# Optimization experiments

Measured on AMD Instinct MI355X. Metric: run time of the kernel, lower is better.

Reference implementation:

```python
import jax, jax.numpy as jnp
import numpy as np

N_NODES = 50000
N_EDGES = 600000
IN_DIM = 128
HID = 128
OUT_DIM = 40
NUM_REL = 3
LN_EPS = 1e-5


def layer_norm(x, g, b):
    mu = jnp.mean(x, axis=-1, keepdims=True)
    var = jnp.var(x, axis=-1, keepdims=True)
    return (x - mu) * jax.lax.rsqrt(var + LN_EPS) * g + b


def rgcn_conv(x, edge_index, edge_type, w_rel, w_root, bias, aggr):
    """PyG-style RGCNConv: out = x @ W_root + bias + sum_r aggr_r(x_src @ W_r)."""
    src, dst = edge_index[0], edge_index[1]
    out = x @ w_root + bias                      # [N, F_out]
    for r in range(NUM_REL):                     # small fixed relation loop
        h = x @ w_rel[r]                         # transform-then-gather: [N, F_out]
        msg = h[src]                             # [E, F_out]
        mask = (edge_type == r)[:, None]
        if aggr == 'add':
            msg = jnp.where(mask, msg, 0.0)
            agg = jax.ops.segment_sum(msg, dst, num_segments=N_NODES)
        else:  # 'max'; empty segments -> 0 (matches PyG scatter_reduce include_self=False over zeros)
            msg = jnp.where(mask, msg, -jnp.inf)
            agg = jax.ops.segment_max(msg, dst, num_segments=N_NODES)
            agg = jnp.where(jnp.isfinite(agg), agg, 0.0)
        out = out + agg
    return out


def setup_inputs() -> dict:
    key = jax.random.key(0)
    ks = jax.random.split(key, 16)
    f32 = jnp.float32
    def lin(k, fan_in, shape):
        return jax.random.normal(k, shape, dtype=f32) / np.sqrt(fan_in)
    inp = {
        'x': jax.random.normal(ks[0], (N_NODES, IN_DIM), dtype=f32),
        'edge_index': jax.random.randint(ks[1], (2, N_EDGES), 0, N_NODES),
        'edge_type': jax.random.randint(ks[2], (N_EDGES,), 0, NUM_REL),
        # conv1
        'w1_rel': lin(ks[3], IN_DIM, (NUM_REL, IN_DIM, HID)),
        'w1_root': lin(ks[4], IN_DIM, (IN_DIM, HID)),
        'b1': jnp.zeros((HID,), f32),
        'ln1_g': jnp.ones((HID,), f32), 'ln1_b': jnp.zeros((HID,), f32),
        # conv2
        'w2_rel': lin(ks[5], HID, (NUM_REL, HID, HID)),
        'w2_root': lin(ks[6], HID, (HID, HID)),
        'b2': jnp.zeros((HID,), f32),
        'ln2_g': jnp.ones((HID,), f32), 'ln2_b': jnp.zeros((HID,), f32),
        # classifier
        'cw1': lin(ks[7], HID, (HID, HID)), 'cb1': jnp.zeros((HID,), f32),
        'cln1_g': jnp.ones((HID,), f32), 'cln1_b': jnp.zeros((HID,), f32),
        'cw2': lin(ks[8], HID, (HID, HID // 2)), 'cb2': jnp.zeros((HID // 2,), f32),
        'cln2_g': jnp.ones((HID // 2,), f32), 'cln2_b': jnp.zeros((HID // 2,), f32),
        'cw3': lin(ks[9], HID // 2, (HID // 2, OUT_DIM)), 'cb3': jnp.zeros((OUT_DIM,), f32),
    }
    return inp


def reference(x, edge_index, edge_type,
              w1_rel, w1_root, b1, ln1_g, ln1_b,
              w2_rel, w2_root, b2, ln2_g, ln2_b,
              cw1, cb1, cln1_g, cln1_b,
              cw2, cb2, cln2_g, cln2_b,
              cw3, cb3):
    # eval mode: edge dropout and feature dropout are identity
    h = rgcn_conv(x, edge_index, edge_type, w1_rel, w1_root, b1, 'add')
    h = jax.nn.relu(layer_norm(h, ln1_g, ln1_b))
    x1 = h
    h = rgcn_conv(x1, edge_index, edge_type, w2_rel, w2_root, b2, 'max')
    h = jax.nn.relu(layer_norm(h, ln2_g, ln2_b))
    h = h + x1 * 0.2
    # classifier MLP
    h = jax.nn.gelu(layer_norm(h @ cw1 + cb1, cln1_g, cln1_b), approximate=False)
    h = jax.nn.gelu(layer_norm(h @ cw2 + cb2, cln2_g, cln2_b), approximate=False)
    h = h @ cw3 + cb3
    return jax.nn.log_softmax(h, axis=1)
```

## Files before the change

### kernel.cpp

```cpp
#include <hip/hip_runtime.h>
#include <hip/hip_bf16.h>
#include <math.h>


typedef __attribute__((ext_vector_type(8))) short bf16x8;
typedef __attribute__((ext_vector_type(4))) float f32x4;
typedef unsigned short ushort_t;

__device__ __forceinline__ ushort_t bf16rne(float v) {
    unsigned u = __float_as_uint(v);
    return (ushort_t)((u + 0x7FFFu + ((u >> 16) & 1u)) >> 16);
}

__device__ __forceinline__ void split_bf16(float v, ushort_t& h, ushort_t& l) {
    ushort_t hu = bf16rne(v);
    float hf = __uint_as_float((unsigned)hu << 16);
    h = hu;
    l = bf16rne(v - hf);
}

__device__ __forceinline__ float bf2f(unsigned u16) {
    return __uint_as_float(u16 << 16);
}

__device__ __forceinline__ float4 unpack_bf4(uint2 u) {
    return make_float4(bf2f(u.x & 0xFFFFu), bf2f(u.x >> 16),
                       bf2f(u.y & 0xFFFFu), bf2f(u.y >> 16));
}

__device__ __forceinline__ uint2 pack_bf4(float4 v) {
    uint2 o;
    o.x = (unsigned)bf16rne(v.x) | ((unsigned)bf16rne(v.y) << 16);
    o.y = (unsigned)bf16rne(v.z) | ((unsigned)bf16rne(v.w) << 16);
    return o;
}

__device__ __forceinline__ void conv_body128(const float* __restrict__ W,
                                             ushort_t* __restrict__ out,
                                             int idx) {
    constexpr int NCF = 8;
    constexpr size_t PST = (size_t)4 * NCF * 512;
    int l = idx & 63;
    int cf = (idx >> 6) & 7;
    int ks = idx >> 9;
    int col = cf * 16 + (l & 15);
    int k0 = ks * 32 + (l >> 4) * 8;
    size_t base = (((size_t)ks * NCF + cf) * 64 + l) * 8;
#pragma unroll
    for (int j = 0; j < 8; ++j) {
        ushort_t h, lo_;
        split_bf16(W[(size_t)(k0 + j) * 128 + col], h, lo_);
        out[base + j] = h;
        out[PST + base + j] = lo_;
    }
}

__global__ __launch_bounds__(256) void convert_all_x2bf(
    const float* __restrict__ w1_root, const float* __restrict__ w1_rel,
    const float* __restrict__ w2_root, const float* __restrict__ w2_rel,
    const float* __restrict__ cw1, const float* __restrict__ cw2,
    ushort_t* __restrict__ wfb,
    const float* __restrict__ x, ushort_t* __restrict__ xh, int n4) {
    int b = blockIdx.x;
    if (b >= 76) {
        int g = (b - 76) * 256 + threadIdx.x;
        if (g < n4) {
            float4 v = ((const float4*)x)[g];
            ((uint2*)xh)[g] = pack_bf4(v);
        }
        return;
    }
    if (b < 72) {
        const float* src;
        int slot;
        if (b < 8)       { slot = 0;              src = w1_root; }
        else if (b < 32) { int r = (b - 8) >> 3;  slot = 1 + r; src = w1_rel + (size_t)r * 16384; }
        else if (b < 40) { slot = 4;              src = w2_root; }
        else if (b < 64) { int r = (b - 40) >> 3; slot = 5 + r; src = w2_rel + (size_t)r * 16384; }
        else             { slot = 8;              src = cw1; }
        int lb = (b < 8) ? b : (b < 32) ? ((b - 8) & 7) : (b < 40) ? (b - 32)
               : (b < 64) ? ((b - 40) & 7) : (b - 64);
        conv_body128(src, wfb + (size_t)slot * 32768, lb * 256 + threadIdx.x);
    } else {
        constexpr int NCF = 4;
        constexpr size_t PST = (size_t)4 * NCF * 512;
        int idx = (b - 72) * 256 + threadIdx.x;
        ushort_t* out = wfb + (size_t)9 * 32768;
        int l = idx & 63;
        int cf = (idx >> 6) & 3;
        int ks = idx >> 8;
        int col = cf * 16 + (l & 15);
        int k0 = ks * 32 + (l >> 4) * 8;
        size_t base = (((size_t)ks * NCF + cf) * 64 + l) * 8;
#pragma unroll
        for (int j = 0; j < 8; ++j) {
            ushort_t h, lo_;
            split_bf16(cw2[(size_t)(k0 + j) * 64 + col], h, lo_);
            out[base + j] = h;
            out[PST + base + j] = lo_;
        }
    }
}

template <int NCOL, int NSEG, int FUSE>
__global__ __launch_bounds__(256, 3) void gemm_bf(
    const ushort_t* __restrict__ A0, const ushort_t* __restrict__ A1,
    const ushort_t* __restrict__ A2, const ushort_t* __restrict__ A3,
    const ushort_t* __restrict__ wfrag, const float* __restrict__ bias,
    const float* __restrict__ lng, const float* __restrict__ lnb,
    void* __restrict__ Yv, int M) {
    constexpr int NCF = NCOL / 16;
    constexpr int WF = NCOL / 32;
    constexpr int PST = 4 * NCF * 512;
    constexpr int WSEG = 2 * PST;
    constexpr int RS = NCOL * 4 + 16;
    constexpr int EPB = 64 * RS;
    constexpr int SMEM_BYTES = (EPB > 16384) ? EPB : 16384;
    __shared__ __align__(16) char smem[SMEM_BYTES];
    char (*lds)[8192] = (char(*)[8192])smem;

    const int tid = threadIdx.x;
    const int wv = tid >> 6, lane = tid & 63, l15 = lane & 15, lg = lane >> 4;
    const int rowgrp = wv >> 1, colgrp = wv & 1;
    const int row0 = blockIdx.x * 64;
    const ushort_t* As[4] = {A0, A1, A2, A3};

    f32x4 acc[2][WF];
#pragma unroll
    for (int xf = 0; xf < 2; ++xf)
#pragma unroll
        for (int wf = 0; wf < WF; ++wf) acc[xf][wf] = (f32x4){0.f, 0.f, 0.f, 0.f};

    uint4 regs[2];

    auto LOADSTAGE = [&](int ch) {
        const ushort_t* __restrict__ A = As[ch >> 1];
        int kcb = (ch & 1) * 128;
#pragma unroll
        for (int i = 0; i < 2; ++i) {
            int s = tid + i * 256;
            int r = s >> 3, c16 = s & 7;
            int gr = row0 + r;
            uint4 v = make_uint4(0u, 0u, 0u, 0u);
            if (gr < M)
                v = *(const uint4*)((const char*)A + (size_t)gr * 256 + kcb + c16 * 16);
            regs[i] = v;
        }
    };

    auto WRITESTAGE = [&](int buf) {
        char* L = lds[buf];
#pragma unroll
        for (int i = 0; i < 2; ++i) {
            int s = tid + i * 256;
            int r = s >> 3, c16 = s & 7;
            int byte = (r * 128 + c16 * 16) ^ ((r & 7) << 4);
            *(uint4*)(L + byte) = regs[i];
        }
    };

    auto COMPUTE = [&](int ch, int buf) {
        int seg = ch >> 1, half = ch & 1;
        const ushort_t* __restrict__ ws = wfrag + (size_t)seg * WSEG;
        const char* L = lds[buf];
#pragma unroll
        for (int kk = 0; kk < 2; ++kk) {
            int ks = half * 2 + kk;
            bf16x8 xh[2];
#pragma unroll
            for (int xf = 0; xf < 2; ++xf) {
                int r = rowgrp * 32 + xf * 16 + l15;
                int byte = (r * 128 + kk * 64 + lg * 16) ^ ((r & 7) << 4);
                xh[xf] = *(const bf16x8*)(L + byte);
            }
            bf16x8 wh[WF], wl[WF];
#pragma unroll
            for (int wf = 0; wf < WF; ++wf) {
                size_t off = (((size_t)ks * NCF + colgrp * WF + wf) * 64 + lane) * 8;
                wh[wf] = *(const bf16x8*)(ws + off);
                wl[wf] = *(const bf16x8*)(ws + PST + off);
            }
#pragma unroll
            for (int xf = 0; xf < 2; ++xf)
#pragma unroll
                for (int wf = 0; wf < WF; ++wf) {
                    acc[xf][wf] = __builtin_amdgcn_mfma_f32_16x16x32_bf16(
                        wh[wf], xh[xf], acc[xf][wf], 0, 0, 0);
                    acc[xf][wf] = __builtin_amdgcn_mfma_f32_16x16x32_bf16(
                        wl[wf], xh[xf], acc[xf][wf], 0, 0, 0);
                }
        }
    };

    constexpr int CH = 2 * NSEG;
    LOADSTAGE(0);
    WRITESTAGE(0);
    __syncthreads();
    for (int ch = 0; ch < CH; ++ch) {
        if (ch + 1 < CH) LOADSTAGE(ch + 1);
        COMPUTE(ch, ch & 1);
        __syncthreads();
        if (ch + 1 < CH) WRITESTAGE((ch + 1) & 1);
        __syncthreads();
    }

    {
        float4 bv[WF];
#pragma unroll
        for (int wf = 0; wf < WF; ++wf) {
            int col = colgrp * (NCOL / 2) + wf * 16 + lg * 4;
            bv[wf] = bias ? *(const float4*)(bias + col)
                          : make_float4(0.f, 0.f, 0.f, 0.f);
        }
#pragma unroll
        for (int xf = 0; xf < 2; ++xf) {
            int r = rowgrp * 32 + xf * 16 + l15;
#pragma unroll
            for (int wf = 0; wf < WF; ++wf) {
                int col = colgrp * (NCOL / 2) + wf * 16 + lg * 4;
                float4 o;
                o.x = acc[xf][wf][0] + bv[wf].x;
                o.y = acc[xf][wf][1] + bv[wf].y;
                o.z = acc[xf][wf][2] + bv[wf].z;
                o.w = acc[xf][wf][3] + bv[wf].w;
                *(float4*)(smem + r * RS + col * 4) = o;
            }
        }
    }
    __syncthreads();

    if (FUSE >= 1 && FUSE <= 3) {
        constexpr int CPT = NCOL / 4;
        int r = tid >> 2, seg = tid & 3;
        char* rp = smem + r * RS + seg * CPT * 4;
        float s = 0.f, sq = 0.f;
        float4 vv[CPT / 4];
#pragma unroll
        for (int j = 0; j < CPT / 4; ++j) {
            float4 v = *(const float4*)(rp + j * 16);
            vv[j] = v;
            s += (v.x + v.y) + (v.z + v.w);
            sq += (v.x * v.x + v.y * v.y) + (v.z * v.z + v.w * v.w);
        }
        s += __shfl_xor(s, 1, 64); sq += __shfl_xor(sq, 1, 64);
        s += __shfl_xor(s, 2, 64); sq += __shfl_xor(sq, 2, 64);
        float mu = s * (1.f / NCOL);
        float var = sq * (1.f / NCOL) - mu * mu;
        float rstd = rsqrtf(var + 1e-5f);
#pragma unroll
        for (int j = 0; j < CPT / 4; ++j) {
            int c0 = seg * CPT + j * 4;
            float4 v = vv[j];
            float4 gg = *(const float4*)(lng + c0);
            float4 bb = *(const float4*)(lnb + c0);
            float y0 = (v.x - mu) * rstd * gg.x + bb.x;
            float y1 = (v.y - mu) * rstd * gg.y + bb.y;
            float y2 = (v.z - mu) * rstd * gg.z + bb.z;
            float y3 = (v.w - mu) * rstd * gg.w + bb.w;
            if (FUSE == 1) {
                y0 = fmaxf(y0, 0.f); y1 = fmaxf(y1, 0.f);
                y2 = fmaxf(y2, 0.f); y3 = fmaxf(y3, 0.f);
            } else {
                y0 = 0.5f * y0 * (1.f + erff(y0 * 0.70710678118654752f));
                y1 = 0.5f * y1 * (1.f + erff(y1 * 0.70710678118654752f));
                y2 = 0.5f * y2 * (1.f + erff(y2 * 0.70710678118654752f));
                y3 = 0.5f * y3 * (1.f + erff(y3 * 0.70710678118654752f));
            }
            vv[j] = make_float4(y0, y1, y2, y3);
        }
        __syncthreads();
        if (FUSE == 3) {
#pragma unroll
            for (int j = 0; j < CPT / 4; ++j) *(float4*)(rp + j * 16) = vv[j];
        } else {
#pragma unroll
            for (int j = 0; j < CPT / 4; ++j) {
                int c0 = seg * CPT + j * 4;
                *(uint2*)(smem + r * RS + 2 * c0) = pack_bf4(vv[j]);
            }
        }
        __syncthreads();
    }

    if (FUSE == 4) {
        constexpr int SL = 64 * (NCOL / 8);
#pragma unroll
        for (int i = 0; i < SL / 256; ++i) {
            int slot = tid + i * 256;
            int rr = slot / (NCOL / 8), c16 = slot % (NCOL / 8);
            int gr = row0 + rr;
            if (gr < M) {
                float4 a = *(const float4*)(smem + rr * RS + c16 * 32);
                float4 b = *(const float4*)(smem + rr * RS + c16 * 32 + 16);
                uint4 o;
                uint2 pa = pack_bf4(a), pb = pack_bf4(b);
                o.x = pa.x; o.y = pa.y; o.z = pb.x; o.w = pb.y;
                *(uint4*)((char*)Yv + (size_t)gr * (NCOL * 2) + c16 * 16) = o;
            }
        }
    } else {
        constexpr int OUTB = (FUSE == 0 || FUSE == 3) ? NCOL * 4 : NCOL * 2;
        constexpr int RP = OUTB / 16;
        constexpr int SL = 64 * RP;
#pragma unroll
        for (int i = 0; i < SL / 256; ++i) {
            int slot = tid + i * 256;
            int rr = slot / RP, c16 = slot % RP;
            int gr = row0 + rr;
            if (gr < M)
                *(uint4*)((char*)Yv + (size_t)gr * OUTB + c16 * 16) =
                    *(const uint4*)(smem + rr * RS + c16 * 16);
        }
    }
}

__global__ __launch_bounds__(256, 3) void gemm_conv2(
    const ushort_t* __restrict__ X, const ushort_t* __restrict__ wfb,
    const float* __restrict__ b2, ushort_t* __restrict__ ACbf,
    ushort_t* __restrict__ H0, ushort_t* __restrict__ H1,
    ushort_t* __restrict__ H2, int M) {
    constexpr int NCF = 8, WF = 4;
    constexpr int PST = 4 * NCF * 512;
    constexpr int RS2 = 256 + 16;
    __shared__ __align__(16) char smem[16384 + 64 * RS2];
    char* Xs = smem;
    char* ep = smem + 16384;

    const int tid = threadIdx.x;
    const int wv = tid >> 6, lane = tid & 63, l15 = lane & 15, lg = lane >> 4;
    const int rowgrp = wv >> 1, colgrp = wv & 1;
    const int row0 = blockIdx.x * 64;

#pragma unroll
    for (int i = 0; i < 4; ++i) {
        int s = tid + i * 256;
        int r = s >> 4, c16 = s & 15;
        int gr = row0 + r;
        uint4 v = make_uint4(0u, 0u, 0u, 0u);
        if (gr < M) v = *(const uint4*)((const char*)X + (size_t)gr * 256 + c16 * 16);
        int byte = (r * 256 + c16 * 16) ^ ((r & 7) << 4);
        *(uint4*)(Xs + byte) = v;
    }
    __syncthreads();

    ushort_t* outs[4] = {ACbf, H0, H1, H2};
    for (int set = 0; set < 4; ++set) {
        const ushort_t* __restrict__ ws = wfb + (size_t)(4 + set) * 32768;
        f32x4 acc[2][WF];
#pragma unroll
        for (int xf = 0; xf < 2; ++xf)
#pragma unroll
            for (int wf = 0; wf < WF; ++wf) acc[xf][wf] = (f32x4){0.f, 0.f, 0.f, 0.f};
#pragma unroll
        for (int ks = 0; ks < 4; ++ks) {
            bf16x8 xh[2];
#pragma unroll
            for (int xf = 0; xf < 2; ++xf) {
                int r = rowgrp * 32 + xf * 16 + l15;
                int byte = (r * 256 + ks * 64 + lg * 16) ^ ((r & 7) << 4);
                xh[xf] = *(const bf16x8*)(Xs + byte);
            }
            bf16x8 wh[WF], wl[WF];
#pragma unroll
            for (int wf = 0; wf < WF; ++wf) {
                size_t off = (((size_t)ks * NCF + colgrp * WF + wf) * 64 + lane) * 8;
                wh[wf] = *(const bf16x8*)(ws + off);
                wl[wf] = *(const bf16x8*)(ws + PST + off);
            }
#pragma unroll
            for (int xf = 0; xf < 2; ++xf)
#pragma unroll
                for (int wf = 0; wf < WF; ++wf) {
                    acc[xf][wf] = __builtin_amdgcn_mfma_f32_16x16x32_bf16(
                        wh[wf], xh[xf], acc[xf][wf], 0, 0, 0);
                    acc[xf][wf] = __builtin_amdgcn_mfma_f32_16x16x32_bf16(
                        wl[wf], xh[xf], acc[xf][wf], 0, 0, 0);
                }
        }
        __syncthreads();
#pragma unroll
        for (int xf = 0; xf < 2; ++xf) {
            int r = rowgrp * 32 + xf * 16 + l15;
#pragma unroll
            for (int wf = 0; wf < WF; ++wf) {
                int col = colgrp * 64 + wf * 16 + lg * 4;
                float4 o;
                o.x = acc[xf][wf][0];
                o.y = acc[xf][wf][1];
                o.z = acc[xf][wf][2];
                o.w = acc[xf][wf][3];
                if (set == 0) {
                    float4 bv = *(const float4*)(b2 + col);
                    o.x += bv.x; o.y += bv.y; o.z += bv.z; o.w += bv.w;
                }
                *(uint2*)(ep + r * RS2 + col * 2) = pack_bf4(o);
            }
        }
        __syncthreads();
        ushort_t* O = outs[set];
#pragma unroll
        for (int i = 0; i < 4; ++i) {
            int slot = tid + i * 256;
            int rr = slot >> 4, c16 = slot & 15;
            int gr = row0 + rr;
            if (gr < M)
                *(uint4*)((char*)O + (size_t)gr * 256 + c16 * 16) =
                    *(const uint4*)(ep + rr * RS2 + c16 * 16);
        }
    }
}

__global__ __launch_bounds__(256) void hist3_kernel(const int* __restrict__ edst,
                                                    const int* __restrict__ etype,
                                                    int* __restrict__ deg3, int E) {
    int e = blockIdx.x * 256 + threadIdx.x;
    if (e < E) atomicAdd(&deg3[edst[e] * 3 + etype[e]], 1);
}

__global__ __launch_bounds__(256) void scan_deg3(const int* __restrict__ deg3,
                                                 int* __restrict__ out,
                                                 int* __restrict__ sums, int n) {
    __shared__ int s[256];
    int g = blockIdx.x * 256 + threadIdx.x;
    int v = 0;
    if (g < n) v = deg3[g * 3] + deg3[g * 3 + 1] + deg3[g * 3 + 2];
    s[threadIdx.x] = v;
    __syncthreads();
    int acc = v;
    for (int off = 1; off < 256; off <<= 1) {
        int t = (threadIdx.x >= off) ? s[threadIdx.x - off] : 0;
        __syncthreads();
        acc += t;
        s[threadIdx.x] = acc;
        __syncthreads();
    }
    if (g < n) out[g] = acc - v;
    if (threadIdx.x == 255 && sums) sums[blockIdx.x] = acc;
}

__global__ __launch_bounds__(256) void scan_block(const int* __restrict__ in,
                                                  int* __restrict__ out,
                                                  int* __restrict__ sums, int n) {
    __shared__ int s[256];
    int g = blockIdx.x * 256 + threadIdx.x;
    int v = (g < n) ? in[g] : 0;
    s[threadIdx.x] = v;
    __syncthreads();
    int acc = v;
    for (int off = 1; off < 256; off <<= 1) {
        int t = (threadIdx.x >= off) ? s[threadIdx.x - off] : 0;
        __syncthreads();
        acc += t;
        s[threadIdx.x] = acc;
        __syncthreads();
    }
    if (g < n) out[g] = acc - v;
    if (threadIdx.x == 255 && sums) sums[blockIdx.x] = acc;
}

__global__ __launch_bounds__(256) void scan_add_ranges(
    const int* __restrict__ scanned, const int* __restrict__ topex,
    const int* __restrict__ deg3, int4* __restrict__ ranges,
    int* __restrict__ cursor3, int n) {
    int g = blockIdx.x * 256 + threadIdx.x;
    if (g >= n) return;
    int b = scanned[g] + topex[blockIdx.x];
    int d0 = deg3[g * 3], d1 = deg3[g * 3 + 1], d2 = deg3[g * 3 + 2];
    int4 r;
    r.x = b; r.y = b + d0; r.z = b + d0 + d1; r.w = b + d0 + d1 + d2;
    ranges[g] = r;
    cursor3[g * 3] = r.x; cursor3[g * 3 + 1] = r.y; cursor3[g * 3 + 2] = r.z;
}

__global__ __launch_bounds__(256) void fill3_kernel(
    const int* __restrict__ esrc, const int* __restrict__ edst,
    const int* __restrict__ etype, int* __restrict__ cursor3,
    int* __restrict__ colidx, int E) {
    int e = blockIdx.x * 256 + threadIdx.x;
    if (e >= E) return;
    int pos = atomicAdd(&cursor3[edst[e] * 3 + etype[e]], 1);
    colidx[pos] = esrc[e];
}

__global__ __launch_bounds__(256) void agg3_add(
    const ushort_t* __restrict__ xh, const int4* __restrict__ ranges,
    const int* __restrict__ colidx, ushort_t* __restrict__ S0,
    ushort_t* __restrict__ S1, ushort_t* __restrict__ S2, int N) {
    int node = blockIdx.x * 8 + (threadIdx.x >> 5);
    int l = threadIdx.x & 31;
    if (node >= N) return;
    int4 rg = ranges[node];
    float4 a0 = make_float4(0.f, 0.f, 0.f, 0.f);
    float4 a1 = a0, a2 = a0;
    int e = rg.x, end = rg.w;

    auto acc1 = [&](int ee, uint2 u) {
        float4 v = unpack_bf4(u);
        bool i0 = ee < rg.y;
        bool i2 = ee >= rg.z;
        bool i1 = !i0 && !i2;
        a0.x += i0 ? v.x : 0.f; a0.y += i0 ? v.y : 0.f;
        a0.z += i0 ? v.z : 0.f; a0.w += i0 ? v.w : 0.f;
        a1.x += i1 ? v.x : 0.f; a1.y += i1 ? v.y : 0.f;
        a1.z += i1 ? v.z : 0.f; a1.w += i1 ? v.w : 0.f;
        a2.x += i2 ? v.x : 0.f; a2.y += i2 ? v.y : 0.f;
        a2.z += i2 ? v.z : 0.f; a2.w += i2 ? v.w : 0.f;
    };

    for (; e + 8 <= end; e += 8) {
        int s[8];
#pragma unroll
        for (int k = 0; k < 8; ++k) s[k] = colidx[e + k];
        uint2 u[8];
#pragma unroll
        for (int k = 0; k < 8; ++k)
            u[k] = *(const uint2*)(xh + (size_t)s[k] * 128 + l * 4);
#pragma unroll
        for (int k = 0; k < 8; ++k) acc1(e + k, u[k]);
    }
    if (e + 4 <= end) {
        int s[4];
#pragma unroll
        for (int k = 0; k < 4; ++k) s[k] = colidx[e + k];
        uint2 u[4];
#pragma unroll
        for (int k = 0; k < 4; ++k)
            u[k] = *(const uint2*)(xh + (size_t)s[k] * 128 + l * 4);
#pragma unroll
        for (int k = 0; k < 4; ++k) acc1(e + k, u[k]);
        e += 4;
    }
    for (; e < end; ++e)
        acc1(e, *(const uint2*)(xh + (size_t)colidx[e] * 128 + l * 4));

    *(uint2*)(S0 + (size_t)node * 128 + l * 4) = pack_bf4(a0);
    *(uint2*)(S1 + (size_t)node * 128 + l * 4) = pack_bf4(a1);
    *(uint2*)(S2 + (size_t)node * 128 + l * 4) = pack_bf4(a2);
}

__global__ __launch_bounds__(256) void maxagg_ln(
    const ushort_t* __restrict__ Hbase, const int4* __restrict__ ranges,
    const int* __restrict__ colidx, const ushort_t* __restrict__ accbf,
    const ushort_t* __restrict__ resid, const float* __restrict__ g,
    const float* __restrict__ b, ushort_t* __restrict__ outH, int N) {
    int node = blockIdx.x * 8 + (threadIdx.x >> 5);
    int l = threadIdx.x & 31;
    if (node >= N) return;
    int4 rg = ranges[node];
    const float NI = -INFINITY;
    float4 m0 = make_float4(NI, NI, NI, NI);
    float4 m1 = m0, m2 = m0;
    int e = rg.x, end = rg.w;

    auto acc1 = [&](int ee, uint2 u) {
        float4 v = unpack_bf4(u);
        bool i0 = ee < rg.y;
        bool i2 = ee >= rg.z;
        bool i1 = !i0 && !i2;
        m0.x = fmaxf(m0.x, i0 ? v.x : NI); m0.y = fmaxf(m0.y, i0 ? v.y : NI);
        m0.z = fmaxf(m0.z, i0 ? v.z : NI); m0.w = fmaxf(m0.w, i0 ? v.w : NI);
        m1.x = fmaxf(m1.x, i1 ? v.x : NI); m1.y = fmaxf(m1.y, i1 ? v.y : NI);
        m1.z = fmaxf(m1.z, i1 ? v.z : NI); m1.w = fmaxf(m1.w, i1 ? v.w : NI);
        m2.x = fmaxf(m2.x, i2 ? v.x : NI); m2.y = fmaxf(m2.y, i2 ? v.y : NI);
        m2.z = fmaxf(m2.z, i2 ? v.z : NI); m2.w = fmaxf(m2.w, i2 ? v.w : NI);
    };
    auto addr = [&](int ee, int src) {
        int rel = (ee >= rg.y) + (ee >= rg.z);
        return Hbase + ((size_t)rel * N + src) * 128 + l * 4;
    };

    for (; e + 8 <= end; e += 8) {
        int s[8];
#pragma unroll
        for (int k = 0; k < 8; ++k) s[k] = colidx[e + k];
        uint2 u[8];
#pragma unroll
        for (int k = 0; k < 8; ++k) u[k] = *(const uint2*)addr(e + k, s[k]);
#pragma unroll
        for (int k = 0; k < 8; ++k) acc1(e + k, u[k]);
    }
    if (e + 4 <= end) {
        int s[4];
#pragma unroll
        for (int k = 0; k < 4; ++k) s[k] = colidx[e + k];
        uint2 u[4];
#pragma unroll
        for (int k = 0; k < 4; ++k) u[k] = *(const uint2*)(addr(e + k, s[k]));
#pragma unroll
        for (int k = 0; k < 4; ++k) acc1(e + k, u[k]);
        e += 4;
    }
    for (; e < end; ++e) acc1(e, *(const uint2*)addr(e, colidx[e]));

    auto fix = [](float4& m) {
        m.x = (m.x > -3e38f) ? m.x : 0.f;
        m.y = (m.y > -3e38f) ? m.y : 0.f;
        m.z = (m.z > -3e38f) ? m.z : 0.f;
        m.w = (m.w > -3e38f) ? m.w : 0.f;
    };
    fix(m0); fix(m1); fix(m2);

    float4 a = unpack_bf4(*(const uint2*)(accbf + (size_t)node * 128 + l * 4));
    a.x += m0.x + m1.x + m2.x;
    a.y += m0.y + m1.y + m2.y;
    a.z += m0.z + m1.z + m2.z;
    a.w += m0.w + m1.w + m2.w;
    float s = (a.x + a.y) + (a.z + a.w);
    float sq = (a.x * a.x + a.y * a.y) + (a.z * a.z + a.w * a.w);
#pragma unroll
    for (int off = 16; off; off >>= 1) {
        s += __shfl_xor(s, off, 64);
        sq += __shfl_xor(sq, off, 64);
    }
    float mu = s * (1.f / 128.f);
    float var = sq * (1.f / 128.f) - mu * mu;
    float rstd = rsqrtf(var + 1e-5f);
    float4 gg = *(const float4*)(g + l * 4);
    float4 bb = *(const float4*)(b + l * 4);
    float4 rv = unpack_bf4(*(const uint2*)(resid + (size_t)node * 128 + l * 4));
    float4 y;
    y.x = fmaxf((a.x - mu) * rstd * gg.x + bb.x, 0.f) + 0.2f * rv.x;
    y.y = fmaxf((a.y - mu) * rstd * gg.y + bb.y, 0.f) + 0.2f * rv.y;
    y.z = fmaxf((a.z - mu) * rstd * gg.z + bb.z, 0.f) + 0.2f * rv.z;
    y.w = fmaxf((a.w - mu) * rstd * gg.w + bb.w, 0.f) + 0.2f * rv.w;
    *(uint2*)(outH + (size_t)node * 128 + l * 4) = pack_bf4(y);
}

__global__ __launch_bounds__(256) void gemm40_lsm(const float* __restrict__ X,
                                                  const float* __restrict__ W,
                                                  const float* __restrict__ bias,
                                                  float* __restrict__ Y, int M) {
    __shared__ float Xs[64][65];
    __shared__ float Ws[64 * 40];
    __shared__ float Ys[64][41];
    __shared__ float mx_[64], ls_[64];
    const int tid = threadIdx.x;
    const int row0 = blockIdx.x * 64;
    for (int i = tid; i < 64 * 40; i += 256) Ws[i] = W[i];
#pragma unroll
    for (int i = 0; i < 4; ++i) {
        int slot = tid + i * 256;
        int r = slot >> 4, c4 = slot & 15;
        float4 v = make_float4(0.f, 0.f, 0.f, 0.f);
        if (row0 + r < M) v = *(const float4*)(X + (size_t)(row0 + r) * 64 + c4 * 4);
        Xs[r][c4 * 4 + 0] = v.x; Xs[r][c4 * 4 + 1] = v.y;
        Xs[r][c4 * 4 + 2] = v.z; Xs[r][c4 * 4 + 3] = v.w;
    }
    __syncthreads();
    const int row = tid >> 2, cg = (tid & 3) * 10;
    float acc[10];
#pragma unroll
    for (int j = 0; j < 10; ++j) acc[j] = 0.f;
#pragma unroll 8
    for (int k = 0; k < 64; ++k) {
        float xv = Xs[row][k];
#pragma unroll
        for (int j = 0; j < 10; ++j) acc[j] = fmaf(xv, Ws[k * 40 + cg + j], acc[j]);
    }
#pragma unroll
    for (int j = 0; j < 10; ++j) Ys[row][cg + j] = acc[j] + bias[cg + j];
    __syncthreads();
    if (tid < 64) {
        float mx = -INFINITY;
#pragma unroll 8
        for (int c = 0; c < 40; ++c) mx = fmaxf(mx, Ys[tid][c]);
        float sum = 0.f;
#pragma unroll 8
        for (int c = 0; c < 40; ++c) sum += __expf(Ys[tid][c] - mx);
        mx_[tid] = mx;
        ls_[tid] = logf(sum);
    }
    __syncthreads();
#pragma unroll
    for (int i = 0; i < 10; ++i) {
        int slot = tid + i * 256;
        int r = slot / 40, c = slot % 40;
        int gr = row0 + r;
        if (gr < M) Y[(size_t)gr * 40 + c] = Ys[r][c] - mx_[r] - ls_[r];
    }
}

extern "C" void kernel_launch(void* const* d_in, const int* in_sizes, int n_in,
                              void* d_out, int out_size, void* d_ws, size_t ws_size,
                              hipStream_t stream) {
    const float* x       = (const float*)d_in[0];
    const int*   eidx    = (const int*)d_in[1];
    const int*   etype   = (const int*)d_in[2];
    const float* w1_rel  = (const float*)d_in[3];
    const float* w1_root = (const float*)d_in[4];
    const float* b1      = (const float*)d_in[5];
    const float* ln1_g   = (const float*)d_in[6];
    const float* ln1_b   = (const float*)d_in[7];
    const float* w2_rel  = (const float*)d_in[8];
    const float* w2_root = (const float*)d_in[9];
    const float* b2      = (const float*)d_in[10];
    const float* ln2_g   = (const float*)d_in[11];
    const float* ln2_b   = (const float*)d_in[12];
    const float* cw1     = (const float*)d_in[13];
    const float* cb1     = (const float*)d_in[14];
    const float* cln1_g  = (const float*)d_in[15];
    const float* cln1_b  = (const float*)d_in[16];
    const float* cw2     = (const float*)d_in[17];
    const float* cb2     = (const float*)d_in[18];
    const float* cln2_g  = (const float*)d_in[19];
    const float* cln2_b  = (const float*)d_in[20];
    const float* cw3     = (const float*)d_in[21];
    const float* cb3     = (const float*)d_in[22];

    const int N = in_sizes[0] / 128;
    const int E = in_sizes[1] / 2;
    const int* esrc = eidx;
    const int* edst = eidx + E;

    const size_t HB = (size_t)N * 256;
    char* base = (char*)d_ws;
    ushort_t* S0 = (ushort_t*)(base + 0 * HB);
    ushort_t* S1 = (ushort_t*)(base + 1 * HB);
    ushort_t* S2 = (ushort_t*)(base + 2 * HB);
    ushort_t* X1 = (ushort_t*)(base + 3 * HB);
    ushort_t* AC = (ushort_t*)(base + 4 * HB);
    char*     B3 = base + 5 * HB;

    int* rowptr  = (int*)B3;
    int* deg3    = rowptr + (N + 1);
    int* cursor3 = deg3 + 3 * N;
    int* bsums   = cursor3 + 3 * N;
    int* btop    = bsums + 256;
    int4* ranges = (int4*)(((uintptr_t)(btop + 256) + 15) & ~(uintptr_t)15);
    int* colidx  = (int*)(ranges + N);
    ushort_t* wfb = (ushort_t*)(((uintptr_t)(colidx + E) + 255) & ~(uintptr_t)255);
    auto WSLOT = [&](int i) { return wfb + (size_t)i * 32768; };
    ushort_t* xh = (ushort_t*)(((uintptr_t)(wfb + 10 * 32768) + 255) & ~(uintptr_t)255);
    ushort_t* h2 = xh;
    ushort_t* C1 = S0;
    float*    C2 = (float*)S1;

    const dim3 blk(256);
    const int gGemm = (N + 63) / 64;
    const int gAgg  = (N + 7) / 8;
    const int gEdge = (E + 255) / 256;
    const int nScanB = (N + 255) / 256;
    const int gX2  = (N * 32 + 255) / 256;

    hipMemsetAsync(deg3, 0, (size_t)3 * N * sizeof(int), stream);
    hist3_kernel<<<gEdge, blk, 0, stream>>>(edst, etype, deg3, E);
    scan_deg3<<<nScanB, blk, 0, stream>>>(deg3, rowptr, bsums, N);
    scan_block<<<1, blk, 0, stream>>>(bsums, btop, nullptr, nScanB);
    scan_add_ranges<<<nScanB, blk, 0, stream>>>(rowptr, btop, deg3, ranges,
                                                cursor3, N);
    fill3_kernel<<<gEdge, blk, 0, stream>>>(esrc, edst, etype, cursor3, colidx, E);

    convert_all_x2bf<<<76 + gX2, blk, 0, stream>>>(
        w1_root, w1_rel, w2_root, w2_rel, cw1, cw2, wfb, x, xh, N * 32);

    agg3_add<<<gAgg, blk, 0, stream>>>(xh, ranges, colidx, S0, S1, S2, N);
    gemm_bf<128, 4, 1><<<gGemm, blk, 0, stream>>>(
        xh, S0, S1, S2, WSLOT(0), b1, ln1_g, ln1_b, X1, N);

    gemm_conv2<<<gGemm, blk, 0, stream>>>(X1, wfb, b2, AC, S0, S1, S2, N);
    maxagg_ln<<<gAgg, blk, 0, stream>>>(S0, ranges, colidx, AC,
                                        X1, ln2_g, ln2_b, h2, N);

    gemm_bf<128, 1, 2><<<gGemm, blk, 0, stream>>>(
        h2, h2, h2, h2, WSLOT(8), cb1, cln1_g, cln1_b, C1, N);
    gemm_bf<64, 1, 3><<<gGemm, blk, 0, stream>>>(
        C1, C1, C1, C1, WSLOT(9), cb2, cln2_g, cln2_b, C2, N);
    gemm40_lsm<<<gGemm, blk, 0, stream>>>(C2, cw3, cb3, (float*)d_out, N);
}
```

Baseline: 257.7 us.

## Use full-wavefront per node with segment-boundary accumulators in aggregation kernels

Both edge aggregation kernels now assign one 64-lane wavefront per node instead of 32 lanes. Each lane handles 2 features with 4-byte gathers instead of 4 features with 8-byte gathers. The per-edge three-way predicated accumulation is replaced by a single running accumulator that is flushed when the edge index crosses the relation boundaries, which cuts ALU work per edge. The trade-off is twice as many threads per node and narrower memory transactions per lane, plus a wider shuffle reduction for the layer norm.

```diff
diff --git a/kernel.cpp b/kernel.cpp
--- a/kernel.cpp
+++ b/kernel.cpp
@@ -28,11 +28,20 @@
                        bf2f(u.y & 0xFFFFu), bf2f(u.y >> 16));
 }
 
+__device__ __forceinline__ float2 unpack_bf2(unsigned u) {
+    return make_float2(__uint_as_float(u << 16),
+                       __uint_as_float(u & 0xFFFF0000u));
+}
+
 __device__ __forceinline__ uint2 pack_bf4(float4 v) {
     uint2 o;
     o.x = (unsigned)bf16rne(v.x) | ((unsigned)bf16rne(v.y) << 16);
     o.y = (unsigned)bf16rne(v.z) | ((unsigned)bf16rne(v.w) << 16);
     return o;
+}
+
+__device__ __forceinline__ unsigned pack_bf2(float2 v) {
+    return (unsigned)bf16rne(v.x) | ((unsigned)bf16rne(v.y) << 16);
 }
 
 __device__ __forceinline__ void conv_body128(const float* __restrict__ W,
@@ -486,56 +495,54 @@
     const ushort_t* __restrict__ xh, const int4* __restrict__ ranges,
     const int* __restrict__ colidx, ushort_t* __restrict__ S0,
     ushort_t* __restrict__ S1, ushort_t* __restrict__ S2, int N) {
-    int node = blockIdx.x * 8 + (threadIdx.x >> 5);
-    int l = threadIdx.x & 31;
+    int node = blockIdx.x * 4 + (threadIdx.x >> 6);
+    int lane = threadIdx.x & 63;
     if (node >= N) return;
     int4 rg = ranges[node];
-    float4 a0 = make_float4(0.f, 0.f, 0.f, 0.f);
-    float4 a1 = a0, a2 = a0;
+    float2 acur = make_float2(0.f, 0.f);
+    float2 a0 = acur, a1 = acur;
     int e = rg.x, end = rg.w;
 
-    auto acc1 = [&](int ee, uint2 u) {
-        float4 v = unpack_bf4(u);
-        bool i0 = ee < rg.y;
-        bool i2 = ee >= rg.z;
-        bool i1 = !i0 && !i2;
-        a0.x += i0 ? v.x : 0.f; a0.y += i0 ? v.y : 0.f;
-        a0.z += i0 ? v.z : 0.f; a0.w += i0 ? v.w : 0.f;
-        a1.x += i1 ? v.x : 0.f; a1.y += i1 ? v.y : 0.f;
-        a1.z += i1 ? v.z : 0.f; a1.w += i1 ? v.w : 0.f;
-        a2.x += i2 ? v.x : 0.f; a2.y += i2 ? v.y : 0.f;
-        a2.z += i2 ? v.z : 0.f; a2.w += i2 ? v.w : 0.f;
+    auto step = [&](int ee, unsigned u) {
+        if (ee == rg.y) { a0 = acur; acur = make_float2(0.f, 0.f); }
+        if (ee == rg.z) { a1 = acur; acur = make_float2(0.f, 0.f); }
+        float2 v = unpack_bf2(u);
+        acur.x += v.x; acur.y += v.y;
     };
 
     for (; e + 8 <= end; e += 8) {
         int s[8];
 #pragma unroll
         for (int k = 0; k < 8; ++k) s[k] = colidx[e + k];
-        uint2 u[8];
+        unsigned u[8];
 #pragma unroll
         for (int k = 0; k < 8; ++k)
-            u[k] = *(const uint2*)(xh + (size_t)s[k] * 128 + l * 4);
-#pragma unroll
-        for (int k = 0; k < 8; ++k) acc1(e + k, u[k]);
+            u[k] = *(const unsigned*)(xh + (size_t)s[k] * 128 + lane * 2);
+#pragma unroll
+        for (int k = 0; k < 8; ++k) step(e + k, u[k]);
     }
     if (e + 4 <= end) {
         int s[4];
 #pragma unroll
         for (int k = 0; k < 4; ++k) s[k] = colidx[e + k];
-        uint2 u[4];
+        unsigned u[4];
 #pragma unroll
         for (int k = 0; k < 4; ++k)
-            u[k] = *(const uint2*)(xh + (size_t)s[k] * 128 + l * 4);
-#pragma unroll
-        for (int k = 0; k < 4; ++k) acc1(e + k, u[k]);
+            u[k] = *(const unsigned*)(xh + (size_t)s[k] * 128 + lane * 2);
+#pragma unroll
+        for (int k = 0; k < 4; ++k) step(e + k, u[k]);
         e += 4;
     }
     for (; e < end; ++e)
-        acc1(e, *(const uint2*)(xh + (size_t)colidx[e] * 128 + l * 4));
-
-    *(uint2*)(S0 + (size_t)node * 128 + l * 4) = pack_bf4(a0);
-    *(uint2*)(S1 + (size_t)node * 128 + l * 4) = pack_bf4(a1);
-    *(uint2*)(S2 + (size_t)node * 128 + l * 4) = pack_bf4(a2);
+        step(e, *(const unsigned*)(xh + (size_t)colidx[e] * 128 + lane * 2));
+
+    if (rg.y == end) { a0 = acur; acur = make_float2(0.f, 0.f); }
+    if (rg.z == end) { a1 = acur; acur = make_float2(0.f, 0.f); }
+    float2 a2 = acur;
+
+    *(unsigned*)(S0 + (size_t)node * 128 + lane * 2) = pack_bf2(a0);
+    *(unsigned*)(S1 + (size_t)node * 128 + lane * 2) = pack_bf2(a1);
+    *(unsigned*)(S2 + (size_t)node * 128 + lane * 2) = pack_bf2(a2);
 }
 
 __global__ __launch_bounds__(256) void maxagg_ln(
@@ -543,87 +550,80 @@
     const int* __restrict__ colidx, const ushort_t* __restrict__ accbf,
     const ushort_t* __restrict__ resid, const float* __restrict__ g,
     const float* __restrict__ b, ushort_t* __restrict__ outH, int N) {
-    int node = blockIdx.x * 8 + (threadIdx.x >> 5);
-    int l = threadIdx.x & 31;
+    int node = blockIdx.x * 4 + (threadIdx.x >> 6);
+    int lane = threadIdx.x & 63;
     if (node >= N) return;
     int4 rg = ranges[node];
     const float NI = -INFINITY;
-    float4 m0 = make_float4(NI, NI, NI, NI);
-    float4 m1 = m0, m2 = m0;
+    float2 mcur = make_float2(NI, NI);
+    float2 m0 = mcur, m1 = mcur;
     int e = rg.x, end = rg.w;
 
-    auto acc1 = [&](int ee, uint2 u) {
-        float4 v = unpack_bf4(u);
-        bool i0 = ee < rg.y;
-        bool i2 = ee >= rg.z;
-        bool i1 = !i0 && !i2;
-        m0.x = fmaxf(m0.x, i0 ? v.x : NI); m0.y = fmaxf(m0.y, i0 ? v.y : NI);
-        m0.z = fmaxf(m0.z, i0 ? v.z : NI); m0.w = fmaxf(m0.w, i0 ? v.w : NI);
-        m1.x = fmaxf(m1.x, i1 ? v.x : NI); m1.y = fmaxf(m1.y, i1 ? v.y : NI);
-        m1.z = fmaxf(m1.z, i1 ? v.z : NI); m1.w = fmaxf(m1.w, i1 ? v.w : NI);
-        m2.x = fmaxf(m2.x, i2 ? v.x : NI); m2.y = fmaxf(m2.y, i2 ? v.y : NI);
-        m2.z = fmaxf(m2.z, i2 ? v.z : NI); m2.w = fmaxf(m2.w, i2 ? v.w : NI);
+    auto step = [&](int ee, unsigned u) {
+        if (ee == rg.y) { m0 = mcur; mcur = make_float2(NI, NI); }
+        if (ee == rg.z) { m1 = mcur; mcur = make_float2(NI, NI); }
+        float2 v = unpack_bf2(u);
+        mcur.x = fmaxf(mcur.x, v.x);
+        mcur.y = fmaxf(mcur.y, v.y);
     };
     auto addr = [&](int ee, int src) {
         int rel = (ee >= rg.y) + (ee >= rg.z);
-        return Hbase + ((size_t)rel * N + src) * 128 + l * 4;
+        return (const unsigned*)(Hbase + ((size_t)rel * N + src) * 128 + lane * 2);
     };
 
     for (; e + 8 <= end; e += 8) {
         int s[8];
 #pragma unroll
         for (int k = 0; k < 8; ++k) s[k] = colidx[e + k];
-        uint2 u[8];
-#pragma unroll
-        for (int k = 0; k < 8; ++k) u[k] = *(const uint2*)addr(e + k, s[k]);
-#pragma unroll
-        for (int k = 0; k < 8; ++k) acc1(e + k, u[k]);
+        unsigned u[8];
+#pragma unroll
+        for (int k = 0; k < 8; ++k) u[k] = *addr(e + k, s[k]);
+#pragma unroll
+        for (int k = 0; k < 8; ++k) step(e + k, u[k]);
     }
     if (e + 4 <= end) {
         int s[4];
 #pragma unroll
         for (int k = 0; k < 4; ++k) s[k] = colidx[e + k];
-        uint2 u[4];
-#pragma unroll
-        for (int k = 0; k < 4; ++k) u[k] = *(const uint2*)(addr(e + k, s[k]));
-#pragma unroll
-        for (int k = 0; k < 4; ++k) acc1(e + k, u[k]);
+        unsigned u[4];
+#pragma unroll
+        for (int k = 0; k < 4; ++k) u[k] = *addr(e + k, s[k]);
+#pragma unroll
+        for (int k = 0; k < 4; ++k) step(e + k, u[k]);
         e += 4;
     }
-    for (; e < end; ++e) acc1(e, *(const uint2*)addr(e, colidx[e]));
-
-    auto fix = [](float4& m) {
+    for (; e < end; ++e) step(e, *addr(e, colidx[e]));
+
+    if (rg.y == end) { m0 = mcur; mcur = make_float2(NI, NI); }
+    if (rg.z == end) { m1 = mcur; mcur = make_float2(NI, NI); }
+    float2 m2 = mcur;
+
+    auto fix = [](float2& m) {
         m.x = (m.x > -3e38f) ? m.x : 0.f;
         m.y = (m.y > -3e38f) ? m.y : 0.f;
-        m.z = (m.z > -3e38f) ? m.z : 0.f;
-        m.w = (m.w > -3e38f) ? m.w : 0.f;
     };
     fix(m0); fix(m1); fix(m2);
 
-    float4 a = unpack_bf4(*(const uint2*)(accbf + (size_t)node * 128 + l * 4));
+    float2 a = unpack_bf2(*(const unsigned*)(accbf + (size_t)node * 128 + lane * 2));
     a.x += m0.x + m1.x + m2.x;
     a.y += m0.y + m1.y + m2.y;
-    a.z += m0.z + m1.z + m2.z;
-    a.w += m0.w + m1.w + m2.w;
-    float s = (a.x + a.y) + (a.z + a.w);
-    float sq = (a.x * a.x + a.y * a.y) + (a.z * a.z + a.w * a.w);
-#pragma unroll
-    for (int off = 16; off; off >>= 1) {
+    float s = a.x + a.y;
+    float sq = a.x * a.x + a.y * a.y;
+#pragma unroll
+    for (int off = 32; off; off >>= 1) {
         s += __shfl_xor(s, off, 64);
         sq += __shfl_xor(sq, off, 64);
     }
     float mu = s * (1.f / 128.f);
     float var = sq * (1.f / 128.f) - mu * mu;
     float rstd = rsqrtf(var + 1e-5f);
-    float4 gg = *(const float4*)(g + l * 4);
-    float4 bb = *(const float4*)(b + l * 4);
-    float4 rv = unpack_bf4(*(const uint2*)(resid + (size_t)node * 128 + l * 4));
-    float4 y;
+    float2 gg = *(const float2*)(g + lane * 2);
+    float2 bb = *(const float2*)(b + lane * 2);
+    float2 rv = unpack_bf2(*(const unsigned*)(resid + (size_t)node * 128 + lane * 2));
+    float2 y;
     y.x = fmaxf((a.x - mu) * rstd * gg.x + bb.x, 0.f) + 0.2f * rv.x;
     y.y = fmaxf((a.y - mu) * rstd * gg.y + bb.y, 0.f) + 0.2f * rv.y;
-    y.z = fmaxf((a.z - mu) * rstd * gg.z + bb.z, 0.f) + 0.2f * rv.z;
-    y.w = fmaxf((a.w - mu) * rstd * gg.w + bb.w, 0.f) + 0.2f * rv.w;
-    *(uint2*)(outH + (size_t)node * 128 + l * 4) = pack_bf4(y);
+    *(unsigned*)(outH + (size_t)node * 128 + lane * 2) = pack_bf2(y);
 }
 
 __global__ __launch_bounds__(256) void gemm40_lsm(const float* __restrict__ X,
@@ -737,7 +737,7 @@
 
     const dim3 blk(256);
     const int gGemm = (N + 63) / 64;
-    const int gAgg  = (N + 7) / 8;
+    const int gAgg4 = (N + 3) / 4;
     const int gEdge = (E + 255) / 256;
     const int nScanB = (N + 255) / 256;
     const int gX2  = (N * 32 + 255) / 256;
@@ -753,13 +753,13 @@
     convert_all_x2bf<<<76 + gX2, blk, 0, stream>>>(
         w1_root, w1_rel, w2_root, w2_rel, cw1, cw2, wfb, x, xh, N * 32);
 
-    agg3_add<<<gAgg, blk, 0, stream>>>(xh, ranges, colidx, S0, S1, S2, N);
+    agg3_add<<<gAgg4, blk, 0, stream>>>(xh, ranges, colidx, S0, S1, S2, N);
     gemm_bf<128, 4, 1><<<gGemm, blk, 0, stream>>>(
         xh, S0, S1, S2, WSLOT(0), b1, ln1_g, ln1_b, X1, N);
 
     gemm_conv2<<<gGemm, blk, 0, stream>>>(X1, wfb, b2, AC, S0, S1, S2, N);
-    maxagg_ln<<<gAgg, blk, 0, stream>>>(S0, ranges, colidx, AC,
-                                        X1, ln2_g, ln2_b, h2, N);
+    maxagg_ln<<<gAgg4, blk, 0, stream>>>(S0, ranges, colidx, AC,
+                                         X1, ln2_g, ln2_b, h2, N);
 
     gemm_bf<128, 1, 2><<<gGemm, blk, 0, stream>>>(
         h2, h2, h2, h2, WSLOT(8), cb1, cln1_g, cln1_b, C1, N);
```

Result: no change. 262.7 us (+1.9%).
